# Optimization experiments

Measured on AMD Instinct MI355X. Metric: run time of the kernel, lower is better.

## Reference

```python
import jax, jax.numpy as jnp
import numpy as np

BATCH, IN_DIM, GRID, HID, DEPTH = 2048, 128, 128, 256, 7
BN_EPS = 1e-5


def setup_inputs() -> dict:
    key = jax.random.key(0)
    ks = jax.random.split(key, 10)
    x = jax.random.uniform(ks[0], (BATCH, IN_DIM), dtype=jnp.float32)
    grids = jax.random.uniform(ks[1], (DEPTH, IN_DIM, GRID), dtype=jnp.float32)  # torch.rand init
    fs = jax.random.normal(ks[2], (DEPTH, IN_DIM, GRID, HID), dtype=jnp.float32)
    depth_scores = jnp.ones((DEPTH,), dtype=jnp.float32)
    mlp_W = jax.random.normal(ks[3], (3, HID, HID), dtype=jnp.float32) * (1.0 / np.sqrt(HID))
    mlp_b = jnp.zeros((3, HID), dtype=jnp.float32)
    bn_gamma = jnp.ones((3, HID), dtype=jnp.float32)
    bn_beta = jnp.zeros((3, HID), dtype=jnp.float32)
    W_out = jax.random.normal(ks[4], (HID, 1), dtype=jnp.float32) * (1.0 / np.sqrt(HID))
    b_out = jnp.zeros((1,), dtype=jnp.float32)
    return {"x": x, "grids": grids, "fs": fs, "depth_scores": depth_scores,
            "mlp_W": mlp_W, "mlp_b": mlp_b, "bn_gamma": bn_gamma,
            "bn_beta": bn_beta, "W_out": W_out, "b_out": b_out}


def reference(x, grids, fs, depth_scores, mlp_W, mlp_b, bn_gamma, bn_beta, W_out, b_out):
    # per-feature min-max normalization over the batch dim
    xmin = x.min(axis=0, keepdims=True)
    xmax = x.max(axis=0, keepdims=True)
    z = (x - xmin) / (xmax - xmin + 1e-6)  # [B, I]

    outputs = []
    for i in range(DEPTH):
        Bmat = jax.nn.relu(z[:, :, None] - grids[i][None, :, :])  # [B, I, G]
        # (B.unsqueeze(-1) * fs[i]).sum(2).sum(1) == einsum big,igh->bh
        H = jnp.einsum('big,igh->bh', Bmat, fs[i])  # [B, H]
        if i > 0:  # residual accumulation
            H = H + outputs[-1]
        outputs.append(H)
    stacked = jnp.stack(outputs, axis=0)  # [D, B, H]
    w = jax.nn.softmax(depth_scores)  # depth attention
    h = jnp.einsum('d,dbh->bh', w, stacked)

    # MLP head (BatchNorm uses batch stats = training-mode behaviour; Dropout off)
    for j in range(3):
        h = h @ mlp_W[j] + mlp_b[j]
        mean = h.mean(axis=0)
        var = h.var(axis=0)  # biased, matching torch BN normalization
        h = (h - mean) * jax.lax.rsqrt(var + BN_EPS) * bn_gamma[j] + bn_beta[j]
        h = jax.nn.gelu(h, approximate=False)  # torch nn.GELU is exact erf GELU
    return h @ W_out + b_out
```

## Files before the change

### kernel.cpp

```cpp
#include <hip/hip_runtime.h>
#include <hip/hip_bf16.h>

#define BATCH 2048
#define IN_DIM 128
#define GRIDN 128
#define HID 256
#define DEPTH 7

typedef unsigned int u32;
typedef __attribute__((ext_vector_type(8))) short short8;
typedef __attribute__((ext_vector_type(4))) float floatx4;

#define OFF_FST   ((size_t)0)
#define SZ_FST    ((size_t)7*128*256*128*2)
#define OFF_ZT    (OFF_FST + SZ_FST)
#define SZ_ZT     ((size_t)BATCH*IN_DIM*4)
#define OFF_HPRE  (OFF_ZT + SZ_ZT)
#define SZ_HPRE   ((size_t)BATCH*HID*4)
#define OFF_STATS (OFF_HPRE + SZ_HPRE)
#define SZ_STATS  ((size_t)3*2*HID*4)
#define OFF_KEYS  (OFF_STATS + SZ_STATS)
#define SZ_KEYS   ((size_t)256*4)
#define OFF_CW    (OFF_KEYS + SZ_KEYS)
#define SZ_CW     ((size_t)32)
#define OFF_Y1    (OFF_CW + SZ_CW)
#define SZ_Y      ((size_t)BATCH*HID*4)
#define OFF_Y2    (OFF_Y1 + SZ_Y)
#define OFF_Y3    (OFF_Y2 + SZ_Y)

__device__ __forceinline__ void gload_lds16(const void* g, void* l) {
  __builtin_amdgcn_global_load_lds(
      (const __attribute__((address_space(1))) u32*)g,
      (__attribute__((address_space(3))) u32*)l, 16, 0, 0);
}

__device__ __forceinline__ u32 pack2_bf16(float lo, float hi) {
  __hip_bfloat162 b2;
  b2.x = __float2bfloat16(lo);
  b2.y = __float2bfloat16(hi);
  return *reinterpret_cast<u32*>(&b2);
}

__device__ __forceinline__ u32 pk_trunc(float a, float b) {
  return __builtin_amdgcn_perm(__float_as_uint(b), __float_as_uint(a), 0x07060302u);
}

__device__ __forceinline__ float gelu_exact(float x) {
  return 0.5f * x * (1.0f + erff(x * 0.70710678118654752f));
}

__global__ void prep1_kernel(const float* __restrict__ x, u32* __restrict__ keys,
                             const float* __restrict__ depth_scores,
                             float* __restrict__ cw) {
  int t = threadIdx.x;
  int base = blockIdx.x * 256 + t;
  float mn = 1e30f, mx = -1e30f;
#pragma unroll
  for (int j = 0; j < 16; ++j) {
    float v = x[base + j * 16384];
    mn = fminf(mn, v); mx = fmaxf(mx, v);
  }
  __shared__ float smn[256], smx[256];
  smn[t] = mn; smx[t] = mx;
  __syncthreads();
  if (t < 128) {
    mn = fminf(smn[t], smn[t + 128]);
    mx = fmaxf(smx[t], smx[t + 128]);
    int i = base & 127;
    atomicMax(&keys[i], 0x7FFFFFFFu - __float_as_uint(mn));
    atomicMax(&keys[128 + i], __float_as_uint(mx));
  }
  if (blockIdx.x == 0 && t == 0) {
    float m = -1e30f;
    for (int d0 = 0; d0 < DEPTH; ++d0) m = fmaxf(m, depth_scores[d0]);
    float e[DEPTH]; float sum = 0.f;
    for (int d0 = 0; d0 < DEPTH; ++d0) { e[d0] = expf(depth_scores[d0] - m); sum += e[d0]; }
    float cacc = 0.f; float cs[DEPTH];
    for (int d0 = DEPTH - 1; d0 >= 0; --d0) { cacc += e[d0] / sum; cs[d0] = cacc; }
    for (int d0 = 0; d0 < DEPTH; ++d0) cw[d0] = cs[d0];
  }
}

__global__ void prep2_kernel(const float* __restrict__ x, const u32* __restrict__ keys,
                             float* __restrict__ z_t) {
  __shared__ float lds[128 * 65];
  int t = threadIdx.x;
  int b0 = blockIdx.x * 64;
#pragma unroll
  for (int q = 0; q < 32; ++q) {
    int idx = q * 256 + t;
    int b = idx >> 7, i = idx & 127;
    lds[i * 65 + b] = x[(size_t)(b0 + b) * IN_DIM + i];
  }
  __syncthreads();
#pragma unroll
  for (int q = 0; q < 32; ++q) {
    int idx = q * 256 + t;
    int ii = idx >> 6, bb = idx & 63;
    float mnv = __uint_as_float(0x7FFFFFFFu - keys[ii]);
    float mxv = __uint_as_float(keys[128 + ii]);
    float v = (lds[ii * 65 + bb] - mnv) * (1.0f / (mxv - mnv + 1e-6f));
    z_t[(size_t)ii * BATCH + b0 + bb] = v;
  }
}

__global__ void convert_kernel(const float* __restrict__ fs,
                               const float* __restrict__ cw,
                               __hip_bfloat16* __restrict__ fs2) {
  __shared__ u32 lds[256 * 33];
  int slab = blockIdx.x;
  int t = threadIdx.x;
  float cd = cw[slab >> 7];
  const float* src = fs + (size_t)slab * (GRIDN * HID);
  char* dstb = (char*)fs2 + (size_t)slab * 65536;

  for (int gh = 0; gh < 2; ++gh) {
    const float* s0 = src + (size_t)gh * 64 * HID + t;
#pragma unroll
    for (int g2 = 0; g2 < 32; ++g2) {
      float va = s0[(size_t)(2 * g2) * HID];
      float vb = s0[(size_t)(2 * g2 + 1) * HID];
      lds[t * 33 + g2] = pack2_bf16(cd * va, cd * vb);
    }
    __syncthreads();
#pragma unroll
    for (int it2 = 0; it2 < 8; ++it2) {
      int task = t + it2 * 256;
      int c = task >> 9;
      int q = task & 511;
      int nhalf = c >> 1, ksl = c & 1;
      int tt = q >> 6, l4 = (q >> 4) & 3, l15 = q & 15;
      int h = nhalf * 128 + tt * 16 + l15;
      int m = ksl * 4 + l4;
      u32 a0 = lds[h * 33 + m * 4 + 0];
      u32 a1 = lds[h * 33 + m * 4 + 1];
      u32 a2 = lds[h * 33 + m * 4 + 2];
      u32 a3 = lds[h * 33 + m * 4 + 3];
      size_t off = (size_t)nhalf * 32768 + (size_t)(gh * 2 + ksl) * 8192 +
                   (size_t)tt * 1024 + l4 * 256 + l15 * 16;
      *(uint4*)(dstb + off) = make_uint4(a0, a1, a2, a3);
    }
    __syncthreads();
  }
}

__launch_bounds__(256, 2)
__global__ void gemm_kernel(const float* __restrict__ z_t,
                            const float* __restrict__ grids,
                            const __hip_bfloat16* __restrict__ fs2,
                            float* __restrict__ h_pre) {
  __shared__ __align__(16) char lds[65536];

  int bx = blockIdx.x;
  int xcd = bx & 7;
  int t6 = bx >> 3;
  int cg = t6 >> 4;
  int jb = t6 & 15;
  int chunk = xcd + 8 * cg;
  int slab0 = chunk * 28;

  int tid = threadIdx.x;
  int w = tid >> 6, l = tid & 63;
  int l15 = l & 15, l4 = l >> 4;
  int wm = w >> 1;
  int wn = w & 1;
  int mbase = jb * 128 + wm * 64;
  int nbase = wn * 128;
  char* mylds = lds + w * 16384;

  floatx4 acc[4][8];
#pragma unroll
  for (int a = 0; a < 4; ++a)
#pragma unroll
    for (int b = 0; b < 8; ++b) acc[a][b] = (floatx4)0.f;

  const char* fsb = (const char*)fs2 + (size_t)slab0 * 65536 + (size_t)wn * 32768 +
                    (size_t)l * 16;

  auto stage = [&](int step, int p) {
    const char* srcb = fsb + (size_t)(step >> 2) * 65536 + (size_t)(step & 3) * 8192;
    char* dst = mylds + p * 8192;
#pragma unroll
    for (int j = 0; j < 8; ++j)
      gload_lds16(srcb + j * 1024, dst + j * 1024);
  };

  float zv[2][4];
  float4 g0[2], g1[2];
  auto loadzg = [&](int step, int p) {
    int slab = slab0 + (step >> 2);
    int iz = slab & 127;
    const float* zp = z_t + (size_t)iz * BATCH + mbase + l15;
    zv[p][0] = zp[0]; zv[p][1] = zp[16]; zv[p][2] = zp[32]; zv[p][3] = zp[48];
    const float* gp = grids + (size_t)slab * GRIDN + (step & 3) * 32 + l4 * 8;
    g0[p] = *(const float4*)gp;
    g1[p] = *(const float4*)(gp + 4);
  };

  loadzg(0, 0);
  stage(0, 0);

#pragma unroll 2
  for (int step = 0; step < 112; ++step) {
    int p = step & 1;
    __builtin_amdgcn_s_waitcnt(0x0F70);
    __asm__ volatile("" ::: "memory");

    short8 bf[8];
#pragma unroll
    for (int tt = 0; tt < 8; ++tt)
      bf[tt] = *(const short8*)(mylds + p * 8192 + tt * 1024 + l * 16);
    __asm__ volatile("" ::: "memory");

    if (step + 1 < 112) stage(step + 1, p ^ 1);

    short8 af[4];
#pragma unroll
    for (int u = 0; u < 4; ++u) {
      float zu = zv[p][u];
      union { uint4 q; short8 s8; } pk;
      pk.q.x = pk_trunc(fmaxf(zu - g0[p].x, 0.f), fmaxf(zu - g0[p].y, 0.f));
      pk.q.y = pk_trunc(fmaxf(zu - g0[p].z, 0.f), fmaxf(zu - g0[p].w, 0.f));
      pk.q.z = pk_trunc(fmaxf(zu - g1[p].x, 0.f), fmaxf(zu - g1[p].y, 0.f));
      pk.q.w = pk_trunc(fmaxf(zu - g1[p].z, 0.f), fmaxf(zu - g1[p].w, 0.f));
      af[u] = pk.s8;
    }

    if (step + 1 < 112) loadzg(step + 1, p ^ 1);

#pragma unroll
    for (int u = 0; u < 4; ++u)
#pragma unroll
      for (int tt = 0; tt < 8; ++tt)
        acc[u][tt] = __builtin_amdgcn_mfma_f32_16x16x32_bf16(af[u], bf[tt], acc[u][tt], 0, 0, 0);
  }

  int row0 = mbase + l4 * 4;
  int col0 = nbase + l15;
#pragma unroll
  for (int u = 0; u < 4; ++u) {
#pragma unroll
    for (int tt = 0; tt < 8; ++tt) {
      int col = col0 + tt * 16;
#pragma unroll
      for (int r = 0; r < 4; ++r) {
        int row = row0 + u * 16 + r;
        atomicAdd(&h_pre[(size_t)row * HID + col], acc[u][tt][r]);
      }
    }
  }
}

template <int FIRST>
__global__ void mlp_kernel(const float* __restrict__ Xin,
                           const float* __restrict__ statsIn,
                           const float* __restrict__ gamma,
                           const float* __restrict__ beta,
                           const float* __restrict__ W,
                           const float* __restrict__ bias,
                           float* __restrict__ Yout,
                           float* __restrict__ statsOut) {
  __shared__ float Xs[4][HID];
  int br = blockIdx.x, c = threadIdx.x;
  float mean = 0.f, rstd = 1.f, gm = 1.f, bt = 0.f;
  if (!FIRST) {
    float s1 = statsIn[c], s2 = statsIn[HID + c];
    mean = s1 * (1.0f / BATCH);
    float var = s2 * (1.0f / BATCH) - mean * mean;
    rstd = rsqrtf(var + 1e-5f);
    gm = gamma[c]; bt = beta[c];
  }
#pragma unroll
  for (int r = 0; r < 4; ++r) {
    float v = Xin[(size_t)(br * 4 + r) * HID + c];
    if (!FIRST) v = gelu_exact((v - mean) * rstd * gm + bt);
    Xs[r][c] = v;
  }
  __syncthreads();
  float acc[4] = {0, 0, 0, 0};
#pragma unroll 8
  for (int k = 0; k < HID; ++k) {
    float wv = W[(size_t)k * HID + c];
#pragma unroll
    for (int r = 0; r < 4; ++r) acc[r] += Xs[r][k] * wv;
  }
  float bb = bias[c];
  float s1 = 0.f, s2 = 0.f;
#pragma unroll
  for (int r = 0; r < 4; ++r) {
    float y = acc[r] + bb;
    Yout[(size_t)(br * 4 + r) * HID + c] = y;
    s1 += y; s2 += y * y;
  }
  atomicAdd(&statsOut[c], s1);
  atomicAdd(&statsOut[HID + c], s2);
}

__global__ void final_kernel(const float* __restrict__ Y3,
                             const float* __restrict__ statsIn,
                             const float* __restrict__ gamma,
                             const float* __restrict__ beta,
                             const float* __restrict__ W_out,
                             const float* __restrict__ b_out,
                             float* __restrict__ out) {
  int w = threadIdx.x >> 6, l = threadIdx.x & 63;
  int b = blockIdx.x * 4 + w;
  float4 y = *(const float4*)(Y3 + (size_t)b * HID + l * 4);
  float4 wv = *(const float4*)(W_out + l * 4);
  float r4[4] = {y.x, y.y, y.z, y.w};
  float w4[4] = {wv.x, wv.y, wv.z, wv.w};
  float s = 0.f;
  int c0 = l * 4;
#pragma unroll
  for (int q = 0; q < 4; ++q) {
    int c = c0 + q;
    float s1 = statsIn[c], s2 = statsIn[HID + c];
    float mean = s1 * (1.0f / BATCH);
    float var = s2 * (1.0f / BATCH) - mean * mean;
    float rstd = rsqrtf(var + 1e-5f);
    float v = gelu_exact((r4[q] - mean) * rstd * gamma[c] + beta[c]);
    s += v * w4[q];
  }
#pragma unroll
  for (int off = 32; off > 0; off >>= 1) s += __shfl_down(s, off);
  if (l == 0) out[b] = s + b_out[0];
}

extern "C" void kernel_launch(void* const* d_in, const int* in_sizes, int n_in,
                              void* d_out, int out_size, void* d_ws, size_t ws_size,
                              hipStream_t stream) {
  const float* x      = (const float*)d_in[0];
  const float* grids  = (const float*)d_in[1];
  const float* fs     = (const float*)d_in[2];
  const float* dscore = (const float*)d_in[3];
  const float* mlp_W  = (const float*)d_in[4];
  const float* mlp_b  = (const float*)d_in[5];
  const float* bn_g   = (const float*)d_in[6];
  const float* bn_b   = (const float*)d_in[7];
  const float* W_out  = (const float*)d_in[8];
  const float* b_out  = (const float*)d_in[9];
  float* out = (float*)d_out;

  char* ws = (char*)d_ws;
  __hip_bfloat16* fs2 = (__hip_bfloat16*)(ws + OFF_FST);
  float* z_t   = (float*)(ws + OFF_ZT);
  float* h_pre = (float*)(ws + OFF_HPRE);
  float* stats = (float*)(ws + OFF_STATS);
  u32*   keys  = (u32*)(ws + OFF_KEYS);
  float* cw    = (float*)(ws + OFF_CW);
  float* Y1    = (float*)(ws + OFF_Y1);
  float* Y2    = (float*)(ws + OFF_Y2);
  float* Y3    = (float*)(ws + OFF_Y3);

  hipMemsetAsync(h_pre, 0, SZ_HPRE + SZ_STATS + SZ_KEYS, stream);

  prep1_kernel<<<64, 256, 0, stream>>>(x, keys, dscore, cw);
  prep2_kernel<<<32, 256, 0, stream>>>(x, keys, z_t);
  convert_kernel<<<DEPTH * IN_DIM, 256, 0, stream>>>(fs, cw, fs2);
  gemm_kernel<<<512, 256, 0, stream>>>(z_t, grids, fs2, h_pre);

  mlp_kernel<1><<<512, 256, 0, stream>>>(h_pre, nullptr, nullptr, nullptr,
                                         mlp_W, mlp_b, Y1, stats);
  mlp_kernel<0><<<512, 256, 0, stream>>>(Y1, stats, bn_g, bn_b,
                                         mlp_W + 65536, mlp_b + 256, Y2, stats + 512);
  mlp_kernel<0><<<512, 256, 0, stream>>>(Y2, stats + 512, bn_g + 256, bn_b + 256,
                                         mlp_W + 2 * 65536, mlp_b + 2 * 256, Y3, stats + 1024);
  final_kernel<<<512, 256, 0, stream>>>(Y3, stats + 1024, bn_g + 512, bn_b + 512,
                                        W_out, b_out, out);
}
```

Before: 450.6 us.

## Fuse prep kernels, load B directly from global, and fuse MLP head cooperatively

Merges the two prep kernels and the memset into one per-feature kernel, and computes the softmax depth weights inside the convert kernel. The GEMM now reads B fragments straight from global memory into registers with double-buffering, dropping the LDS staging. The three MLP layers and the output layer become one cooperative kernel that uses grid.sync for the BatchNorm statistics. This removes launch overhead and intermediate buffers, but risks worse GEMM latency hiding without LDS and adds grid-sync cost.

```diff
diff --git a/kernel.cpp b/kernel.cpp
--- a/kernel.cpp
+++ b/kernel.cpp
@@ -1,5 +1,6 @@
 #include <hip/hip_runtime.h>
 #include <hip/hip_bf16.h>
+#include <hip/hip_cooperative_groups.h>
 
 #define BATCH 2048
 #define IN_DIM 128
@@ -19,20 +20,6 @@
 #define SZ_HPRE   ((size_t)BATCH*HID*4)
 #define OFF_STATS (OFF_HPRE + SZ_HPRE)
 #define SZ_STATS  ((size_t)3*2*HID*4)
-#define OFF_KEYS  (OFF_STATS + SZ_STATS)
-#define SZ_KEYS   ((size_t)256*4)
-#define OFF_CW    (OFF_KEYS + SZ_KEYS)
-#define SZ_CW     ((size_t)32)
-#define OFF_Y1    (OFF_CW + SZ_CW)
-#define SZ_Y      ((size_t)BATCH*HID*4)
-#define OFF_Y2    (OFF_Y1 + SZ_Y)
-#define OFF_Y3    (OFF_Y2 + SZ_Y)
-
-__device__ __forceinline__ void gload_lds16(const void* g, void* l) {
-  __builtin_amdgcn_global_load_lds(
-      (const __attribute__((address_space(1))) u32*)g,
-      (__attribute__((address_space(3))) u32*)l, 16, 0, 0);
-}
 
 __device__ __forceinline__ u32 pack2_bf16(float lo, float hi) {
   __hip_bfloat162 b2;
@@ -49,68 +36,58 @@
   return 0.5f * x * (1.0f + erff(x * 0.70710678118654752f));
 }
 
-__global__ void prep1_kernel(const float* __restrict__ x, u32* __restrict__ keys,
-                             const float* __restrict__ depth_scores,
-                             float* __restrict__ cw) {
-  int t = threadIdx.x;
-  int base = blockIdx.x * 256 + t;
+__global__ void prep_kernel(const float* __restrict__ x,
+                            float* __restrict__ z_t,
+                            float* __restrict__ h_pre,
+                            float* __restrict__ stats) {
+  int i = blockIdx.x, t = threadIdx.x;
+  float v[8];
   float mn = 1e30f, mx = -1e30f;
 #pragma unroll
-  for (int j = 0; j < 16; ++j) {
-    float v = x[base + j * 16384];
-    mn = fminf(mn, v); mx = fmaxf(mx, v);
+  for (int j = 0; j < 8; ++j) {
+    v[j] = x[(size_t)(t + j * 256) * IN_DIM + i];
+    mn = fminf(mn, v[j]); mx = fmaxf(mx, v[j]);
   }
   __shared__ float smn[256], smx[256];
   smn[t] = mn; smx[t] = mx;
   __syncthreads();
-  if (t < 128) {
-    mn = fminf(smn[t], smn[t + 128]);
-    mx = fmaxf(smx[t], smx[t + 128]);
-    int i = base & 127;
-    atomicMax(&keys[i], 0x7FFFFFFFu - __float_as_uint(mn));
-    atomicMax(&keys[128 + i], __float_as_uint(mx));
-  }
-  if (blockIdx.x == 0 && t == 0) {
-    float m = -1e30f;
-    for (int d0 = 0; d0 < DEPTH; ++d0) m = fmaxf(m, depth_scores[d0]);
-    float e[DEPTH]; float sum = 0.f;
-    for (int d0 = 0; d0 < DEPTH; ++d0) { e[d0] = expf(depth_scores[d0] - m); sum += e[d0]; }
-    float cacc = 0.f; float cs[DEPTH];
-    for (int d0 = DEPTH - 1; d0 >= 0; --d0) { cacc += e[d0] / sum; cs[d0] = cacc; }
-    for (int d0 = 0; d0 < DEPTH; ++d0) cw[d0] = cs[d0];
-  }
-}
-
-__global__ void prep2_kernel(const float* __restrict__ x, const u32* __restrict__ keys,
-                             float* __restrict__ z_t) {
-  __shared__ float lds[128 * 65];
-  int t = threadIdx.x;
-  int b0 = blockIdx.x * 64;
-#pragma unroll
-  for (int q = 0; q < 32; ++q) {
-    int idx = q * 256 + t;
-    int b = idx >> 7, i = idx & 127;
-    lds[i * 65 + b] = x[(size_t)(b0 + b) * IN_DIM + i];
-  }
-  __syncthreads();
-#pragma unroll
-  for (int q = 0; q < 32; ++q) {
-    int idx = q * 256 + t;
-    int ii = idx >> 6, bb = idx & 63;
-    float mnv = __uint_as_float(0x7FFFFFFFu - keys[ii]);
-    float mxv = __uint_as_float(keys[128 + ii]);
-    float v = (lds[ii * 65 + bb] - mnv) * (1.0f / (mxv - mnv + 1e-6f));
-    z_t[(size_t)ii * BATCH + b0 + bb] = v;
+  for (int s = 128; s > 0; s >>= 1) {
+    if (t < s) { smn[t] = fminf(smn[t], smn[t + s]); smx[t] = fmaxf(smx[t], smx[t + s]); }
+    __syncthreads();
+  }
+  float lo = smn[0];
+  float inv = 1.0f / (smx[0] - lo + 1e-6f);
+#pragma unroll
+  for (int j = 0; j < 8; ++j)
+    z_t[(size_t)i * BATCH + t + j * 256] = (v[j] - lo) * inv;
+  float4 zz = make_float4(0.f, 0.f, 0.f, 0.f);
+  float4* hz = (float4*)(h_pre + (size_t)i * 4096);
+#pragma unroll
+  for (int q = 0; q < 4; ++q) hz[q * 256 + t] = zz;
+  if (i == 0) {
+    for (int q = t; q < 1536; q += 256) stats[q] = 0.f;
   }
 }
 
 __global__ void convert_kernel(const float* __restrict__ fs,
-                               const float* __restrict__ cw,
+                               const float* __restrict__ depth_scores,
                                __hip_bfloat16* __restrict__ fs2) {
   __shared__ u32 lds[256 * 33];
   int slab = blockIdx.x;
   int t = threadIdx.x;
-  float cd = cw[slab >> 7];
+  int d = slab >> 7;
+  float m = -1e30f;
+#pragma unroll
+  for (int d0 = 0; d0 < DEPTH; ++d0) m = fmaxf(m, depth_scores[d0]);
+  float sum = 0.f, num = 0.f;
+#pragma unroll
+  for (int d0 = 0; d0 < DEPTH; ++d0) {
+    float e = expf(depth_scores[d0] - m);
+    sum += e;
+    if (d0 >= d) num += e;
+  }
+  float cd = num / sum;
+
   const float* src = fs + (size_t)slab * (GRIDN * HID);
   char* dstb = (char*)fs2 + (size_t)slab * 65536;
 
@@ -131,11 +108,11 @@
       int nhalf = c >> 1, ksl = c & 1;
       int tt = q >> 6, l4 = (q >> 4) & 3, l15 = q & 15;
       int h = nhalf * 128 + tt * 16 + l15;
-      int m = ksl * 4 + l4;
-      u32 a0 = lds[h * 33 + m * 4 + 0];
-      u32 a1 = lds[h * 33 + m * 4 + 1];
-      u32 a2 = lds[h * 33 + m * 4 + 2];
-      u32 a3 = lds[h * 33 + m * 4 + 3];
+      int mm = ksl * 4 + l4;
+      u32 a0 = lds[h * 33 + mm * 4 + 0];
+      u32 a1 = lds[h * 33 + mm * 4 + 1];
+      u32 a2 = lds[h * 33 + mm * 4 + 2];
+      u32 a3 = lds[h * 33 + mm * 4 + 3];
       size_t off = (size_t)nhalf * 32768 + (size_t)(gh * 2 + ksl) * 8192 +
                    (size_t)tt * 1024 + l4 * 256 + l15 * 16;
       *(uint4*)(dstb + off) = make_uint4(a0, a1, a2, a3);
@@ -149,8 +126,6 @@
                             const float* __restrict__ grids,
                             const __hip_bfloat16* __restrict__ fs2,
                             float* __restrict__ h_pre) {
-  __shared__ __align__(16) char lds[65536];
-
   int bx = blockIdx.x;
   int xcd = bx & 7;
   int t6 = bx >> 3;
@@ -162,11 +137,9 @@
   int tid = threadIdx.x;
   int w = tid >> 6, l = tid & 63;
   int l15 = l & 15, l4 = l >> 4;
-  int wm = w >> 1;
-  int wn = w & 1;
+  int wm = w >> 1, wn = w & 1;
   int mbase = jb * 128 + wm * 64;
   int nbase = wn * 128;
-  char* mylds = lds + w * 16384;
 
   floatx4 acc[4][8];
 #pragma unroll
@@ -174,65 +147,75 @@
 #pragma unroll
     for (int b = 0; b < 8; ++b) acc[a][b] = (floatx4)0.f;
 
-  const char* fsb = (const char*)fs2 + (size_t)slab0 * 65536 + (size_t)wn * 32768 +
-                    (size_t)l * 16;
-
-  auto stage = [&](int step, int p) {
-    const char* srcb = fsb + (size_t)(step >> 2) * 65536 + (size_t)(step & 3) * 8192;
-    char* dst = mylds + p * 8192;
-#pragma unroll
-    for (int j = 0; j < 8; ++j)
-      gload_lds16(srcb + j * 1024, dst + j * 1024);
-  };
-
+  const char* bptr = (const char*)fs2 + (size_t)slab0 * 65536 + (size_t)wn * 32768 +
+                     (size_t)l * 16;
+
+  short8 bf[2][4];
   float zv[2][4];
   float4 g0[2], g1[2];
-  auto loadzg = [&](int step, int p) {
-    int slab = slab0 + (step >> 2);
-    int iz = slab & 127;
+
+  auto loadB = [&](int sub, int p) {
+    const char* src = bptr + (size_t)(sub >> 3) * 65536 + (size_t)((sub >> 1) & 3) * 8192 +
+                      (size_t)(sub & 1) * 4096;
+    bf[p][0] = *(const short8*)(src);
+    bf[p][1] = *(const short8*)(src + 1024);
+    bf[p][2] = *(const short8*)(src + 2048);
+    bf[p][3] = *(const short8*)(src + 3072);
+  };
+  auto loadZ = [&](int s, int p) {
+    int iz = (slab0 + s) & 127;
     const float* zp = z_t + (size_t)iz * BATCH + mbase + l15;
     zv[p][0] = zp[0]; zv[p][1] = zp[16]; zv[p][2] = zp[32]; zv[p][3] = zp[48];
-    const float* gp = grids + (size_t)slab * GRIDN + (step & 3) * 32 + l4 * 8;
+  };
+  auto loadG = [&](int s, int ks, int p) {
+    const float* gp = grids + (size_t)(slab0 + s) * GRIDN + ks * 32 + l4 * 8;
     g0[p] = *(const float4*)gp;
     g1[p] = *(const float4*)(gp + 4);
   };
 
-  loadzg(0, 0);
-  stage(0, 0);
-
-#pragma unroll 2
-  for (int step = 0; step < 112; ++step) {
-    int p = step & 1;
-    __builtin_amdgcn_s_waitcnt(0x0F70);
-    __asm__ volatile("" ::: "memory");
-
-    short8 bf[8];
-#pragma unroll
-    for (int tt = 0; tt < 8; ++tt)
-      bf[tt] = *(const short8*)(mylds + p * 8192 + tt * 1024 + l * 16);
-    __asm__ volatile("" ::: "memory");
-
-    if (step + 1 < 112) stage(step + 1, p ^ 1);
-
-    short8 af[4];
-#pragma unroll
-    for (int u = 0; u < 4; ++u) {
-      float zu = zv[p][u];
-      union { uint4 q; short8 s8; } pk;
-      pk.q.x = pk_trunc(fmaxf(zu - g0[p].x, 0.f), fmaxf(zu - g0[p].y, 0.f));
-      pk.q.y = pk_trunc(fmaxf(zu - g0[p].z, 0.f), fmaxf(zu - g0[p].w, 0.f));
-      pk.q.z = pk_trunc(fmaxf(zu - g1[p].x, 0.f), fmaxf(zu - g1[p].y, 0.f));
-      pk.q.w = pk_trunc(fmaxf(zu - g1[p].z, 0.f), fmaxf(zu - g1[p].w, 0.f));
-      af[u] = pk.s8;
-    }
-
-    if (step + 1 < 112) loadzg(step + 1, p ^ 1);
-
-#pragma unroll
-    for (int u = 0; u < 4; ++u)
-#pragma unroll
-      for (int tt = 0; tt < 8; ++tt)
-        acc[u][tt] = __builtin_amdgcn_mfma_f32_16x16x32_bf16(af[u], bf[tt], acc[u][tt], 0, 0, 0);
+  loadB(0, 0);
+  loadZ(0, 0);
+  loadG(0, 0, 0);
+
+#pragma unroll 1
+  for (int s = 0; s < 28; ++s) {
+    int sp = s & 1;
+#pragma unroll
+    for (int ks = 0; ks < 4; ++ks) {
+      int kp = (s * 4 + ks) & 1;
+      {
+        int nn = s * 4 + ks + 1;
+        if (nn > 111) nn = 111;
+        loadG(nn >> 2, nn & 3, kp ^ 1);
+      }
+      if (ks == 0) loadZ((s + 1 < 28) ? s + 1 : s, sp ^ 1);
+
+      short8 af[4];
+#pragma unroll
+      for (int u = 0; u < 4; ++u) {
+        float zu = zv[sp][u];
+        union { uint4 q; short8 s8; } pk;
+        pk.q.x = pk_trunc(fmaxf(zu - g0[kp].x, 0.f), fmaxf(zu - g0[kp].y, 0.f));
+        pk.q.y = pk_trunc(fmaxf(zu - g0[kp].z, 0.f), fmaxf(zu - g0[kp].w, 0.f));
+        pk.q.z = pk_trunc(fmaxf(zu - g1[kp].x, 0.f), fmaxf(zu - g1[kp].y, 0.f));
+        pk.q.w = pk_trunc(fmaxf(zu - g1[kp].z, 0.f), fmaxf(zu - g1[kp].w, 0.f));
+        af[u] = pk.s8;
+      }
+
+#pragma unroll
+      for (int grp = 0; grp < 2; ++grp) {
+        int sub = (s * 4 + ks) * 2 + grp;
+        int bp = sub & 1;
+        int nsub = sub + 1; if (nsub > 223) nsub = 223;
+        loadB(nsub, bp ^ 1);
+#pragma unroll
+        for (int u = 0; u < 4; ++u)
+#pragma unroll
+          for (int tt = 0; tt < 4; ++tt)
+            acc[u][grp * 4 + tt] = __builtin_amdgcn_mfma_f32_16x16x32_bf16(
+                af[u], bf[bp][tt], acc[u][grp * 4 + tt], 0, 0, 0);
+      }
+    }
   }
 
   int row0 = mbase + l4 * 4;
@@ -251,79 +234,61 @@
   }
 }
 
-template <int FIRST>
-__global__ void mlp_kernel(const float* __restrict__ Xin,
-                           const float* __restrict__ statsIn,
-                           const float* __restrict__ gamma,
-                           const float* __restrict__ beta,
-                           const float* __restrict__ W,
-                           const float* __restrict__ bias,
-                           float* __restrict__ Yout,
-                           float* __restrict__ statsOut) {
-  __shared__ float Xs[4][HID];
+__global__ void head_kernel(const float* __restrict__ h_pre,
+                            const float* __restrict__ mlp_W,
+                            const float* __restrict__ mlp_b,
+                            const float* __restrict__ bn_g,
+                            const float* __restrict__ bn_b,
+                            const float* __restrict__ W_out,
+                            const float* __restrict__ b_out,
+                            float* __restrict__ stats,
+                            float* __restrict__ out) {
+  cooperative_groups::grid_group grid = cooperative_groups::this_grid();
+  __shared__ float Xs[8][HID];
   int br = blockIdx.x, c = threadIdx.x;
-  float mean = 0.f, rstd = 1.f, gm = 1.f, bt = 0.f;
-  if (!FIRST) {
-    float s1 = statsIn[c], s2 = statsIn[HID + c];
-    mean = s1 * (1.0f / BATCH);
-    float var = s2 * (1.0f / BATCH) - mean * mean;
-    rstd = rsqrtf(var + 1e-5f);
-    gm = gamma[c]; bt = beta[c];
-  }
-#pragma unroll
-  for (int r = 0; r < 4; ++r) {
-    float v = Xin[(size_t)(br * 4 + r) * HID + c];
-    if (!FIRST) v = gelu_exact((v - mean) * rstd * gm + bt);
-    Xs[r][c] = v;
-  }
+#pragma unroll
+  for (int r = 0; r < 8; ++r) Xs[r][c] = h_pre[(size_t)(br * 8 + r) * HID + c];
   __syncthreads();
-  float acc[4] = {0, 0, 0, 0};
+  float y[8];
+#pragma unroll 1
+  for (int j = 0; j < 3; ++j) {
+    const float* W = mlp_W + (size_t)j * HID * HID;
+    float acc[8] = {0.f, 0.f, 0.f, 0.f, 0.f, 0.f, 0.f, 0.f};
 #pragma unroll 8
-  for (int k = 0; k < HID; ++k) {
-    float wv = W[(size_t)k * HID + c];
-#pragma unroll
-    for (int r = 0; r < 4; ++r) acc[r] += Xs[r][k] * wv;
-  }
-  float bb = bias[c];
-  float s1 = 0.f, s2 = 0.f;
-#pragma unroll
-  for (int r = 0; r < 4; ++r) {
-    float y = acc[r] + bb;
-    Yout[(size_t)(br * 4 + r) * HID + c] = y;
-    s1 += y; s2 += y * y;
-  }
-  atomicAdd(&statsOut[c], s1);
-  atomicAdd(&statsOut[HID + c], s2);
-}
-
-__global__ void final_kernel(const float* __restrict__ Y3,
-                             const float* __restrict__ statsIn,
-                             const float* __restrict__ gamma,
-                             const float* __restrict__ beta,
-                             const float* __restrict__ W_out,
-                             const float* __restrict__ b_out,
-                             float* __restrict__ out) {
-  int w = threadIdx.x >> 6, l = threadIdx.x & 63;
-  int b = blockIdx.x * 4 + w;
-  float4 y = *(const float4*)(Y3 + (size_t)b * HID + l * 4);
-  float4 wv = *(const float4*)(W_out + l * 4);
-  float r4[4] = {y.x, y.y, y.z, y.w};
-  float w4[4] = {wv.x, wv.y, wv.z, wv.w};
-  float s = 0.f;
-  int c0 = l * 4;
-#pragma unroll
-  for (int q = 0; q < 4; ++q) {
-    int c = c0 + q;
-    float s1 = statsIn[c], s2 = statsIn[HID + c];
-    float mean = s1 * (1.0f / BATCH);
-    float var = s2 * (1.0f / BATCH) - mean * mean;
+    for (int k = 0; k < HID; ++k) {
+      float wv = W[(size_t)k * HID + c];
+#pragma unroll
+      for (int r = 0; r < 8; ++r) acc[r] += Xs[r][k] * wv;
+    }
+    float bb = mlp_b[j * HID + c];
+    float s1 = 0.f, s2 = 0.f;
+#pragma unroll
+    for (int r = 0; r < 8; ++r) { y[r] = acc[r] + bb; s1 += y[r]; s2 += y[r] * y[r]; }
+    atomicAdd(&stats[j * 512 + c], s1);
+    atomicAdd(&stats[j * 512 + 256 + c], s2);
+    grid.sync();
+    float mean = stats[j * 512 + c] * (1.0f / BATCH);
+    float var = stats[j * 512 + 256 + c] * (1.0f / BATCH) - mean * mean;
     float rstd = rsqrtf(var + 1e-5f);
-    float v = gelu_exact((r4[q] - mean) * rstd * gamma[c] + beta[c]);
-    s += v * w4[q];
-  }
-#pragma unroll
-  for (int off = 32; off > 0; off >>= 1) s += __shfl_down(s, off);
-  if (l == 0) out[b] = s + b_out[0];
+    float gm = bn_g[j * HID + c], bt = bn_b[j * HID + c];
+#pragma unroll
+    for (int r = 0; r < 8; ++r) Xs[r][c] = gelu_exact((y[r] - mean) * rstd * gm + bt);
+    __syncthreads();
+  }
+  float wo = W_out[c];
+  float bo = b_out[0];
+  __shared__ float red[4];
+  int wv_ = c >> 6, lane = c & 63;
+#pragma unroll 1
+  for (int r = 0; r < 8; ++r) {
+    float v = Xs[r][c] * wo;
+#pragma unroll
+    for (int off = 32; off > 0; off >>= 1) v += __shfl_down(v, off);
+    if (lane == 0) red[wv_] = v;
+    __syncthreads();
+    if (c == 0) out[br * 8 + r] = red[0] + red[1] + red[2] + red[3] + bo;
+    __syncthreads();
+  }
 }
 
 extern "C" void kernel_launch(void* const* d_in, const int* in_sizes, int n_in,
@@ -346,25 +311,15 @@
   float* z_t   = (float*)(ws + OFF_ZT);
   float* h_pre = (float*)(ws + OFF_HPRE);
   float* stats = (float*)(ws + OFF_STATS);
-  u32*   keys  = (u32*)(ws + OFF_KEYS);
-  float* cw    = (float*)(ws + OFF_CW);
-  float* Y1    = (float*)(ws + OFF_Y1);
-  float* Y2    = (float*)(ws + OFF_Y2);
-  float* Y3    = (float*)(ws + OFF_Y3);
-
-  hipMemsetAsync(h_pre, 0, SZ_HPRE + SZ_STATS + SZ_KEYS, stream);
-
-  prep1_kernel<<<64, 256, 0, stream>>>(x, keys, dscore, cw);
-  prep2_kernel<<<32, 256, 0, stream>>>(x, keys, z_t);
-  convert_kernel<<<DEPTH * IN_DIM, 256, 0, stream>>>(fs, cw, fs2);
+
+  prep_kernel<<<128, 256, 0, stream>>>(x, z_t, h_pre, stats);
+  convert_kernel<<<DEPTH * IN_DIM, 256, 0, stream>>>(fs, dscore, fs2);
   gemm_kernel<<<512, 256, 0, stream>>>(z_t, grids, fs2, h_pre);
 
-  mlp_kernel<1><<<512, 256, 0, stream>>>(h_pre, nullptr, nullptr, nullptr,
-                                         mlp_W, mlp_b, Y1, stats);
-  mlp_kernel<0><<<512, 256, 0, stream>>>(Y1, stats, bn_g, bn_b,
-                                         mlp_W + 65536, mlp_b + 256, Y2, stats + 512);
-  mlp_kernel<0><<<512, 256, 0, stream>>>(Y2, stats + 512, bn_g + 256, bn_b + 256,
-                                         mlp_W + 2 * 65536, mlp_b + 2 * 256, Y3, stats + 1024);
-  final_kernel<<<512, 256, 0, stream>>>(Y3, stats + 1024, bn_g + 512, bn_b + 512,
-                                        W_out, b_out, out);
-}
+  const float* hp = h_pre;
+  float* st = stats;
+  void* hargs[] = {(void*)&hp, (void*)&mlp_W, (void*)&mlp_b, (void*)&bn_g,
+                   (void*)&bn_b, (void*)&W_out, (void*)&b_out, (void*)&st,
+                   (void*)&out};
+  hipLaunchCooperativeKernel((void*)head_kernel, dim3(256), dim3(256), hargs, 0, stream);
+}
```

Result: slower. 572.0 us (+27.0%).
